# Kernel optimization log

Hardware: AMD Instinct MI355X
Metric: run time of the kernel (lower is better)

## Reference

```python
import jax, jax.numpy as jnp
import numpy as np

N_NODES = 100000
N_EDGES = 3200000
D_IN = 64
D_HID = 64


def _sage_conv(x, src, dst, Wl, bl, Wr, n_nodes):
    # PyG SAGEConv (aggr='mean', root_weight=True):
    #   out = lin_l(mean_{j in N(i)} x_j) + lin_r(x_i)
    msg = x[src]                                              # [E, d] gather
    agg = jax.ops.segment_sum(msg, dst, num_segments=n_nodes) # [N, d] scatter-sum
    cnt = jax.ops.segment_sum(jnp.ones((src.shape[0],), x.dtype), dst,
                              num_segments=n_nodes)           # [N]
    agg = agg / jnp.maximum(cnt, 1.0)[:, None]                # mean (empty -> 0)
    return agg @ Wl.T + bl + x @ Wr.T


def setup_inputs() -> dict:
    key = jax.random.key(0)
    ks = jax.random.split(key, 12)
    x = jax.random.normal(ks[0], (N_NODES, D_IN), dtype=jnp.float32)
    edge_index = jax.random.randint(ks[1], (2, N_EDGES), 0, N_NODES, dtype=jnp.int64)
    s = 1.0 / np.sqrt(D_IN)
    h = 1.0 / np.sqrt(D_HID)
    params = {
        'Wl1': jax.random.uniform(ks[2], (D_HID, D_IN), jnp.float32, -s, s),
        'bl1': jnp.zeros((D_HID,), jnp.float32),
        'Wr1': jax.random.uniform(ks[3], (D_HID, D_IN), jnp.float32, -s, s),
        'Wl2': jax.random.uniform(ks[4], (D_HID, D_HID), jnp.float32, -h, h),
        'bl2': jnp.zeros((D_HID,), jnp.float32),
        'Wr2': jax.random.uniform(ks[5], (D_HID, D_HID), jnp.float32, -h, h),
        'Wl3': jax.random.uniform(ks[6], (D_HID, D_HID), jnp.float32, -h, h),
        'bl3': jnp.zeros((D_HID,), jnp.float32),
        'Wr3': jax.random.uniform(ks[7], (D_HID, D_HID), jnp.float32, -h, h),
        'Wlin': jax.random.uniform(ks[8], (1, D_HID), jnp.float32, -h, h),
        'blin': jnp.zeros((1,), jnp.float32),
    }
    return {'x': x, 'edge_index': edge_index, **params}


def reference(x, edge_index, Wl1, bl1, Wr1, Wl2, bl2, Wr2, Wl3, bl3, Wr3, Wlin, blin):
    src, dst = edge_index[0], edge_index[1]
    n = x.shape[0]
    h = _sage_conv(x, src, dst, Wl1, bl1, Wr1, n)
    h = _sage_conv(h, src, dst, Wl2, bl2, Wr2, n)
    h = _sage_conv(h, src, dst, Wl3, bl3, Wr3, n)
    # global_mean_pool with batch=None -> single graph mean over all nodes
    g = jnp.mean(h, axis=0, keepdims=True)   # [1, D_HID]
    return g @ Wlin.T + blin                 # [1, 1]
```

## Files before the change

kernel.cpp:

```cpp
#include <hip/hip_runtime.h>
#include <stdint.h>

#define D 64
#define PNBLK 512
#define NBMAX 400
#define CAPS 16
#define CAPD 32
#define XPB 512
#define XPST 272

__device__ __forceinline__ uint32_t rup8(uint32_t v) { return (v + 7u) & ~7u; }

__global__ void zero_kernel(float* __restrict__ p, int n) {
    int i = blockIdx.x * blockDim.x + threadIdx.x;
    if (i < n) p[i] = 0.0f;
}

__global__ void cnt_kernel(const int* __restrict__ dst, float* __restrict__ cnt, int ne) {
    int i = blockIdx.x * blockDim.x + threadIdx.x;
    if (i < ne) atomicAdd(&cnt[dst[i]], 1.0f);
}
__global__ void scatter_kernel(const int* __restrict__ src, const int* __restrict__ dst,
                               const float* __restrict__ r, float* __restrict__ an, int ne) {
    int i = blockIdx.x * blockDim.x + threadIdx.x;
    if (i < ne) atomicAdd(&an[src[i]], r[dst[i]]);
}
__global__ void r0_kernel(const float* __restrict__ cnt, float* __restrict__ r, int nn) {
    int i = blockIdx.x * blockDim.x + threadIdx.x;
    if (i < nn) r[i] = (1.0f / (float)nn) / fmaxf(cnt[i], 1.0f);
}
__global__ void rdiv_kernel(const float* __restrict__ a, const float* __restrict__ cnt,
                            float* __restrict__ r, int nn) {
    int i = blockIdx.x * blockDim.x + threadIdx.x;
    if (i < nn) r[i] = a[i] / fmaxf(cnt[i], 1.0f);
}


__global__ __launch_bounds__(512) void hist_kernel(
        const int* __restrict__ src, const int* __restrict__ dst,
        uint32_t* __restrict__ blkhistS, uint32_t* __restrict__ blkhistD,
        int ne, int nb, int chunk) {
    __shared__ uint32_t hS[2][NBMAX], hD[2][NBMAX];
    const int T = blockDim.x, tid = threadIdx.x;
    for (int i = tid; i < nb; i += T) { hS[0][i] = 0u; hS[1][i] = 0u; hD[0][i] = 0u; hD[1][i] = 0u; }
    __syncthreads();
    const int cp = tid & 1;
    int beg = blockIdx.x * chunk;
    int end = min(beg + chunk, ne);
    for (int base = beg; base < end; base += T * 4) {
        int e0 = base + tid * 4;
        if (e0 + 3 < end) {
            int4 s4 = *(const int4*)(src + e0);
            int4 d4 = *(const int4*)(dst + e0);
            atomicAdd(&hS[cp][((uint32_t)s4.x) >> 8], 1u);
            atomicAdd(&hS[cp][((uint32_t)s4.y) >> 8], 1u);
            atomicAdd(&hS[cp][((uint32_t)s4.z) >> 8], 1u);
            atomicAdd(&hS[cp][((uint32_t)s4.w) >> 8], 1u);
            atomicAdd(&hD[cp][((uint32_t)d4.x) >> 8], 1u);
            atomicAdd(&hD[cp][((uint32_t)d4.y) >> 8], 1u);
            atomicAdd(&hD[cp][((uint32_t)d4.z) >> 8], 1u);
            atomicAdd(&hD[cp][((uint32_t)d4.w) >> 8], 1u);
        } else {
            for (int k = 0; k < 4; k++) {
                int e = e0 + k;
                if (e < end) {
                    atomicAdd(&hS[cp][((uint32_t)src[e]) >> 8], 1u);
                    atomicAdd(&hD[cp][((uint32_t)dst[e]) >> 8], 1u);
                }
            }
        }
    }
    __syncthreads();
    for (int i = tid; i < nb; i += T) {
        blkhistS[(size_t)blockIdx.x * nb + i] = hS[0][i] + hS[1][i];
        blkhistD[(size_t)blockIdx.x * nb + i] = hD[0][i] + hD[1][i];
    }
}

__global__ __launch_bounds__(64) void reduce_kernel(
        const uint32_t* __restrict__ blkhistS, const uint32_t* __restrict__ blkhistD,
        uint32_t* __restrict__ totS, uint32_t* __restrict__ totD, int nb) {
    int which = (blockIdx.x >= nb) ? 1 : 0;
    int b = blockIdx.x - which * nb;
    const uint32_t* bh = which ? blkhistD : blkhistS;
    uint32_t* to       = which ? totD : totS;
    int lane = threadIdx.x;
    uint32_t s = 0;
    #pragma unroll
    for (int j = 0; j < PNBLK / 64; j++) {
        uint32_t c = bh[(size_t)(lane + j * 64) * nb + b];
        s += which ? c : rup8(c);
    }
    #pragma unroll
    for (int off = 32; off; off >>= 1) s += __shfl_down(s, off);
    if (lane == 0) to[b] = s;
}

__global__ __launch_bounds__(512) void scan_kernel(
        const uint32_t* __restrict__ totS, const uint32_t* __restrict__ totD,
        uint32_t* __restrict__ bstartS, uint32_t* __restrict__ bstartD,
        float* __restrict__ X, int nb) {
    const int isS = (blockIdx.x == 0);
    const uint32_t* to = isS ? totS : totD;
    uint32_t* bs       = isS ? bstartS : bstartD;
    const int tid = threadIdx.x;
    if (!isS && tid < 4 * D + 2) X[tid] = 0.0f;
    uint32_t tot = (tid < nb) ? to[tid] : 0u;
    int lane = tid & 63, wid = tid >> 6;
    uint32_t incl = tot;
    #pragma unroll
    for (int off = 1; off < 64; off <<= 1) {
        uint32_t nbr = __shfl_up(incl, off, 64);
        if (lane >= off) incl += nbr;
    }
    __shared__ uint32_t wsum[8];
    if (lane == 63) wsum[wid] = incl;
    __syncthreads();
    if (wid == 0 && lane < 8) {
        uint32_t w = wsum[lane], wi = w;
        #pragma unroll
        for (int off = 1; off < 8; off <<= 1) {
            uint32_t nbr = __shfl_up(wi, off, 8);
            if (lane >= off) wi += nbr;
        }
        wsum[lane] = wi - w;
    }
    __syncthreads();
    uint32_t excl = incl - tot + wsum[wid];
    if (tid < nb) bs[tid] = excl;
    if (tid == nb - 1) bs[nb] = excl + tot;
}

__global__ __launch_bounds__(64) void offsets_kernel(
        const uint32_t* __restrict__ blkhistS, const uint32_t* __restrict__ blkhistD,
        const uint32_t* __restrict__ bstartS, const uint32_t* __restrict__ bstartD,
        uint32_t* __restrict__ offsS, uint32_t* __restrict__ offsD, int nb) {
    int which = (blockIdx.x >= nb) ? 1 : 0;
    int b = blockIdx.x - which * nb;
    const uint32_t* bh = which ? blkhistD : blkhistS;
    const uint32_t* bs = which ? bstartD  : bstartS;
    uint32_t* of       = which ? offsD    : offsS;
    int lane = threadIdx.x;
    const int K = PNBLK / 64;
    uint32_t v[K];
    uint32_t s = 0;
    int base = lane * K;
    #pragma unroll
    for (int k = 0; k < K; k++) {
        uint32_t c = bh[(size_t)(base + k) * nb + b];
        v[k] = which ? c : rup8(c);
        s += v[k];
    }
    uint32_t inc = s;
    #pragma unroll
    for (int off = 1; off < 64; off <<= 1) {
        uint32_t nbr = __shfl_up(inc, off, 64);
        if (lane >= off) inc += nbr;
    }
    uint32_t run = bs[b] + (inc - s);
    #pragma unroll
    for (int k = 0; k < K; k++) { of[(size_t)(base + k) * nb + b] = run; run += v[k]; }
}

__global__ __launch_bounds__(512) void place_kernel(
        const int* __restrict__ src, const int* __restrict__ dst,
        const uint32_t* __restrict__ offsS, const uint32_t* __restrict__ offsD,
        uint32_t* __restrict__ sortedS, uint8_t* __restrict__ sortedD,
        int ne, int nb, int chunk, uint32_t sentinel) {
    __shared__ uint32_t stS[NBMAX * CAPS];
    __shared__ uint8_t  stD[NBMAX * CAPD];
    __shared__ uint32_t pendS[NBMAX], pendD[NBMAX];
    __shared__ uint32_t gposS[NBMAX], gposD[NBMAX];
    __shared__ int again;
    const int T = blockDim.x, tid = threadIdx.x;
    for (int i = tid; i < nb; i += T) {
        pendS[i] = 0u; pendD[i] = 0u;
        gposS[i] = offsS[(size_t)blockIdx.x * nb + i];
        gposD[i] = offsD[(size_t)blockIdx.x * nb + i];
    }
    __syncthreads();
    int beg = blockIdx.x * chunk;
    int end = min(beg + chunk, ne);
    for (int base = beg; base < end; base += T * 4) {
        uint32_t vS[4]; uint8_t vD[4]; int bS[4], bD[4]; bool hS[4], hD[4];
        int e0 = base + tid * 4;
        if (e0 + 3 < end) {
            int4 s4 = *(const int4*)(src + e0);
            int4 d4 = *(const int4*)(dst + e0);
            int sv[4] = {s4.x, s4.y, s4.z, s4.w};
            int dv[4] = {d4.x, d4.y, d4.z, d4.w};
            #pragma unroll
            for (int k = 0; k < 4; k++) {
                uint32_t s = (uint32_t)sv[k], d = (uint32_t)dv[k];
                bS[k] = s >> 8; vS[k] = ((s & 255u) << 17) | d;
                bD[k] = d >> 8; vD[k] = (uint8_t)(d & 255u);
                hS[k] = true; hD[k] = true;
            }
        } else {
            #pragma unroll
            for (int k = 0; k < 4; k++) {
                int e = e0 + k;
                bool ok = e < end;
                hS[k] = ok; hD[k] = ok;
                if (ok) {
                    uint32_t s = (uint32_t)src[e], d = (uint32_t)dst[e];
                    bS[k] = s >> 8; vS[k] = ((s & 255u) << 17) | d;
                    bD[k] = d >> 8; vD[k] = (uint8_t)(d & 255u);
                } else { bS[k] = 0; bD[k] = 0; vS[k] = 0; vD[k] = 0; }
            }
        }
        while (true) {
            if (tid == 0) again = 0;
            __syncthreads();
            #pragma unroll
            for (int k = 0; k < 4; k++) {
                if (hS[k]) {
                    uint32_t p = atomicAdd(&pendS[bS[k]], 1u);
                    if (p < CAPS) { stS[bS[k] * CAPS + p] = vS[k]; hS[k] = false; }
                }
                if (hD[k]) {
                    uint32_t p = atomicAdd(&pendD[bD[k]], 1u);
                    if (p < CAPD) { stD[bD[k] * CAPD + p] = vD[k]; hD[k] = false; }
                }
            }
            if (hS[0] | hS[1] | hS[2] | hS[3] | hD[0] | hD[1] | hD[2] | hD[3]) again = 1;
            __syncthreads();
            for (int bb = tid; bb < nb; bb += T) {
                uint32_t n = min(pendS[bb], (uint32_t)CAPS);
                if (n == CAPS) {
                    uint32_t g = gposS[bb];
                    uint4* dstp = (uint4*)(sortedS + g);
                    const uint4* srcp = (const uint4*)(stS + bb * CAPS);
                    dstp[0] = srcp[0]; dstp[1] = srcp[1];
                    dstp[2] = srcp[2]; dstp[3] = srcp[3];
                    gposS[bb] = g + CAPS;
                    pendS[bb] = 0u;
                } else pendS[bb] = n;
                n = min(pendD[bb], (uint32_t)CAPD);
                if (n == CAPD) {
                    uint32_t g = gposD[bb];
                    #pragma unroll
                    for (int k = 0; k < CAPD; k++) sortedD[g + k] = stD[bb * CAPD + k];
                    gposD[bb] = g + CAPD;
                    pendD[bb] = 0u;
                } else pendD[bb] = n;
            }
            __syncthreads();
            const int cont = again;
            __syncthreads();
            if (!cont) break;
        }
    }
    for (int bb = tid; bb < nb; bb += T) {
        uint32_t n = pendS[bb];
        if (n > 0) {
            uint32_t g = gposS[bb];
            uint32_t m = rup8(n);
            uint32_t tmp[CAPS];
            for (uint32_t k = 0; k < m; k++) tmp[k] = (k < n) ? stS[bb * CAPS + k] : sentinel;
            for (uint32_t k = 0; k < m; k += 8) {
                uint4* dstp = (uint4*)(sortedS + g + k);
                dstp[0] = *(const uint4*)(tmp + k);
                dstp[1] = *(const uint4*)(tmp + k + 4);
            }
        }
        uint32_t nD = pendD[bb], gD = gposD[bb];
        for (uint32_t k = 0; k < nD; k++) sortedD[gD + k] = stD[bb * CAPD + k];
    }
}

__global__ __launch_bounds__(512) void cntb_kernel(
        const uint8_t* __restrict__ sortedD, const uint32_t* __restrict__ bstartD,
        float* __restrict__ cnt, float* __restrict__ rA, float* __restrict__ rB,
        int nn, float invN) {
    int b = blockIdx.x, tid = threadIdx.x;
    __shared__ uint32_t c[2][256];
    ((uint32_t*)c)[tid] = 0u;
    __syncthreads();
    const int cp = tid & 1;
    uint32_t beg = bstartD[b], end = bstartD[b + 1];
    for (uint32_t e = beg + tid; e < end; e += 512) atomicAdd(&c[cp][sortedD[e]], 1u);
    __syncthreads();
    if (b == 0 && tid == 0) { rA[nn] = 0.0f; rB[nn] = 0.0f; }
    int v = b * 256 + tid;
    if (tid < 256 && v < nn) {
        float cf = (float)(c[0][tid] + c[1][tid]);
        cnt[v] = cf;
        rA[v] = invN / fmaxf(cf, 1.0f);
    }
}

__global__ __launch_bounds__(512) void scatb_kernel(
        const uint32_t* __restrict__ sortedS, const uint32_t* __restrict__ bstartS,
        const float* __restrict__ rin, const float* __restrict__ cnt,
        float* __restrict__ aout, float* __restrict__ rout, int nn) {
    int b = blockIdx.x, tid = threadIdx.x;
    __shared__ float acc[2][256];
    ((float*)acc)[tid] = 0.0f;
    __syncthreads();
    const int cp = tid & 1;
    uint32_t beg = bstartS[b], end = bstartS[b + 1];
    for (uint32_t e = beg + tid * 4; e < end; e += 512 * 4) {
        uint4 p = *(const uint4*)(sortedS + e);
        atomicAdd(&acc[cp][p.x >> 17], rin[p.x & 0x1FFFFu]);
        atomicAdd(&acc[cp][p.y >> 17], rin[p.y & 0x1FFFFu]);
        atomicAdd(&acc[cp][p.z >> 17], rin[p.z & 0x1FFFFu]);
        atomicAdd(&acc[cp][p.w >> 17], rin[p.w & 0x1FFFFu]);
    }
    __syncthreads();
    int v = b * 256 + tid;
    if (tid < 256 && v < nn) {
        float a = acc[0][tid] + acc[1][tid];
        aout[v] = a;
        if (rout) rout[v] = a / fmaxf(cnt[v], 1.0f);
    }
}

__global__ __launch_bounds__(256) void xpass_kernel(
        const float* __restrict__ x,
        const float* __restrict__ a1, const float* __restrict__ a2,
        const float* __restrict__ a3, float* __restrict__ Xpart, int nn) {
    const int tid = threadIdx.x;
    const int cg = tid & 15;
    const int rs = tid >> 4;
    float4 c0 = {0,0,0,0}, c1 = {0,0,0,0}, c2 = {0,0,0,0}, c3 = {0,0,0,0};
    float ss1 = 0.f, ss2 = 0.f;
    for (int i = blockIdx.x * 16 + rs; i < nn; i += gridDim.x * 16) {
        float4 xv = *(const float4*)(x + (size_t)i * D + cg * 4);
        float w1 = a1[i], w2 = a2[i], w3 = a3[i];
        c0.x += xv.x; c0.y += xv.y; c0.z += xv.z; c0.w += xv.w;
        c1.x = fmaf(w1, xv.x, c1.x); c1.y = fmaf(w1, xv.y, c1.y);
        c1.z = fmaf(w1, xv.z, c1.z); c1.w = fmaf(w1, xv.w, c1.w);
        c2.x = fmaf(w2, xv.x, c2.x); c2.y = fmaf(w2, xv.y, c2.y);
        c2.z = fmaf(w2, xv.z, c2.z); c2.w = fmaf(w2, xv.w, c2.w);
        c3.x = fmaf(w3, xv.x, c3.x); c3.y = fmaf(w3, xv.y, c3.y);
        c3.z = fmaf(w3, xv.z, c3.z); c3.w = fmaf(w3, xv.w, c3.w);
        if (cg == 0) { ss1 += w1; ss2 += w2; }
    }
    __shared__ float4 sm[4][16][16];
    __shared__ float sms1[16], sms2[16];
    sm[0][rs][cg] = c0; sm[1][rs][cg] = c1; sm[2][rs][cg] = c2; sm[3][rs][cg] = c3;
    if (cg == 0) { sms1[rs] = ss1; sms2[rs] = ss2; }
    __syncthreads();
    for (int s = 8; s; s >>= 1) {
        if (rs < s) {
            #pragma unroll
            for (int k = 0; k < 4; k++) {
                float4 a = sm[k][rs][cg], b = sm[k][rs + s][cg];
                a.x += b.x; a.y += b.y; a.z += b.z; a.w += b.w;
                sm[k][rs][cg] = a;
            }
            if (cg == 0) { sms1[rs] += sms1[rs + s]; sms2[rs] += sms2[rs + s]; }
        }
        __syncthreads();
    }
    float* outp = Xpart + (size_t)blockIdx.x * XPST;
    {
        int k = tid >> 6, col = tid & 63;
        outp[tid] = ((const float*)&sm[k][0][col >> 2])[col & 3];
    }
    if (tid == 0) outp[256] = sms1[0];
    if (tid == 1) outp[257] = sms2[0];
}

__global__ __launch_bounds__(64) void xreduce_kernel(
        const float* __restrict__ Xpart, float* __restrict__ X, int nxb) {
    int j = blockIdx.x;
    int lane = threadIdx.x;
    float s = 0.f;
    for (int b = lane; b < nxb; b += 64) s += Xpart[(size_t)b * XPST + j];
    #pragma unroll
    for (int off = 32; off; off >>= 1) s += __shfl_down(s, off);
    if (lane == 0) X[j] = s;
}

__global__ __launch_bounds__(256) void final_kernel(const float* __restrict__ X,
    const float* __restrict__ Wl1, const float* __restrict__ bl1, const float* __restrict__ Wr1,
    const float* __restrict__ Wl2, const float* __restrict__ bl2, const float* __restrict__ Wr2,
    const float* __restrict__ Wl3, const float* __restrict__ bl3, const float* __restrict__ Wr3,
    const float* __restrict__ Wlin, const float* __restrict__ blin,
    float* __restrict__ out, int nn) {
    const int tid = threadIdx.x;
    const int t = tid >> 2, q = tid & 3, c0 = q * 16;
    __shared__ float X1[D], X2[D], X3[D], X4[D];
    __shared__ float m1u[D], m1a1[D], m1a2[D], m2u[D], m2a1[D];
    __shared__ float sred[4];
    if (tid < 64)       X1[tid]       = X[tid] * (1.0f / (float)nn);
    else if (tid < 128) X2[tid - 64]  = X[tid];
    else if (tid < 192) X3[tid - 128] = X[tid];
    else                X4[tid - 192] = X[tid];
    const float s1 = X[4 * D], s2 = X[4 * D + 1];
    __syncthreads();

    float dl2 = 0.f, dl3 = 0.f, dl4 = 0.f, dr1 = 0.f, dr2 = 0.f, dr3 = 0.f;
    #pragma unroll
    for (int k = 0; k < 16; k++) {
        int c = c0 + k;
        float wl = Wl1[t * D + c], wr = Wr1[t * D + c];
        dl2 = fmaf(wl, X2[c], dl2); dl3 = fmaf(wl, X3[c], dl3); dl4 = fmaf(wl, X4[c], dl4);
        dr1 = fmaf(wr, X1[c], dr1); dr2 = fmaf(wr, X2[c], dr2); dr3 = fmaf(wr, X3[c], dr3);
    }
    #define RED4(v) { v += __shfl_down(v, 2, 4); v += __shfl_down(v, 1, 4); }
    RED4(dl2) RED4(dl3) RED4(dl4) RED4(dr1) RED4(dr2) RED4(dr3)
    if (q == 0) {
        m1u[t]  = dl2 + bl1[t]      + dr1;
        m1a1[t] = dl3 + bl1[t] * s1 + dr2;
        m1a2[t] = dl4 + bl1[t] * s2 + dr3;
    }
    __syncthreads();

    float el1 = 0.f, el2 = 0.f, er0 = 0.f, er1 = 0.f;
    #pragma unroll
    for (int k = 0; k < 16; k++) {
        int c = c0 + k;
        float wl = Wl2[t * D + c], wr = Wr2[t * D + c];
        el1 = fmaf(wl, m1a1[c], el1); el2 = fmaf(wl, m1a2[c], el2);
        er0 = fmaf(wr, m1u[c],  er0); er1 = fmaf(wr, m1a1[c], er1);
    }
    RED4(el1) RED4(el2) RED4(er0) RED4(er1)
    if (q == 0) {
        m2u[t]  = el1 + bl2[t]      + er0;
        m2a1[t] = el2 + bl2[t] * s1 + er1;
    }
    __syncthreads();

    float fl = 0.f, fr = 0.f;
    #pragma unroll
    for (int k = 0; k < 16; k++) {
        int c = c0 + k;
        fl = fmaf(Wl3[t * D + c], m2a1[c], fl);
        fr = fmaf(Wr3[t * D + c], m2u[c],  fr);
    }
    RED4(fl) RED4(fr)
    float contrib = 0.f;
    if (q == 0) contrib = Wlin[t] * (fl + bl3[t] + fr);
    #pragma unroll
    for (int off = 32; off; off >>= 1) contrib += __shfl_down(contrib, off);
    if ((tid & 63) == 0) sred[tid >> 6] = contrib;
    __syncthreads();
    if (tid == 0) out[0] = sred[0] + sred[1] + sred[2] + sred[3] + blin[0];
}

extern "C" void kernel_launch(void* const* d_in, const int* in_sizes, int n_in,
                              void* d_out, int out_size, void* d_ws, size_t ws_size,
                              hipStream_t stream) {
    const float* x    = (const float*)d_in[0];
    const int*   ei   = (const int*)d_in[1];
    const float* Wl1  = (const float*)d_in[2];
    const float* bl1  = (const float*)d_in[3];
    const float* Wr1  = (const float*)d_in[4];
    const float* Wl2  = (const float*)d_in[5];
    const float* bl2  = (const float*)d_in[6];
    const float* Wr2  = (const float*)d_in[7];
    const float* Wl3  = (const float*)d_in[8];
    const float* bl3  = (const float*)d_in[9];
    const float* Wr3  = (const float*)d_in[10];
    const float* Wlin = (const float*)d_in[11];
    const float* blin = (const float*)d_in[12];
    float* out = (float*)d_out;

    const int nn = in_sizes[0] / D;
    const int ne = in_sizes[1] / 2;
    const int* srcIdx = ei;
    const int* dstIdx = ei + ne;
    const int nb = (nn + 255) >> 8;

    char* base = (char*)d_ws;
    size_t cur = 0;
    auto alloc = [&](size_t bytes) -> void* {
        void* p = base + cur;
        cur = (cur + bytes + 255) & ~(size_t)255;
        return p;
    };
    float*    cnt      = (float*)alloc((size_t)nn * 4);
    float*    a1       = (float*)alloc((size_t)nn * 4);
    float*    a2       = (float*)alloc((size_t)nn * 4);
    float*    a3       = (float*)alloc((size_t)nn * 4);
    float*    rA       = (float*)alloc((size_t)(nn + 1) * 4);
    float*    rB       = (float*)alloc((size_t)(nn + 1) * 4);
    float*    X        = (float*)alloc((4 * D + 2) * 4);
    float*    Xpart    = (float*)alloc((size_t)XPB * XPST * 4);
    size_t    zend     = cur;
    uint32_t* blkhistS = (uint32_t*)alloc((size_t)PNBLK * nb * 4);
    uint32_t* blkhistD = (uint32_t*)alloc((size_t)PNBLK * nb * 4);
    uint32_t* offsS    = (uint32_t*)alloc((size_t)PNBLK * nb * 4);
    uint32_t* offsD    = (uint32_t*)alloc((size_t)PNBLK * nb * 4);
    uint32_t* bstartS  = (uint32_t*)alloc((size_t)(nb + 1) * 4);
    uint32_t* bstartD  = (uint32_t*)alloc((size_t)(nb + 1) * 4);
    uint32_t* totS     = (uint32_t*)alloc((size_t)nb * 4);
    uint32_t* totD     = (uint32_t*)alloc((size_t)nb * 4);
    uint32_t* sortedS  = (uint32_t*)alloc(((size_t)ne + (size_t)PNBLK * nb * 7) * 4);
    uint8_t*  sortedD  = (uint8_t*)alloc((size_t)ne);
    const size_t need = cur;

    const int B = 256;
    if (need <= ws_size && nn <= 131071 && nb <= NBMAX) {
        const int chunk = ((ne + PNBLK - 1) / PNBLK + 3) & ~3;
        hipLaunchKernelGGL(hist_kernel, dim3(PNBLK), dim3(512), 0, stream,
                           srcIdx, dstIdx, blkhistS, blkhistD, ne, nb, chunk);
        hipLaunchKernelGGL(reduce_kernel, dim3(2 * nb), dim3(64), 0, stream,
                           blkhistS, blkhistD, totS, totD, nb);
        hipLaunchKernelGGL(scan_kernel, dim3(2), dim3(512), 0, stream,
                           totS, totD, bstartS, bstartD, X, nb);
        hipLaunchKernelGGL(offsets_kernel, dim3(2 * nb), dim3(64), 0, stream,
                           blkhistS, blkhistD, bstartS, bstartD, offsS, offsD, nb);
        hipLaunchKernelGGL(place_kernel, dim3(PNBLK), dim3(512), 0, stream,
                           srcIdx, dstIdx, offsS, offsD, sortedS, sortedD, ne, nb, chunk,
                           (uint32_t)nn);
        hipLaunchKernelGGL(cntb_kernel, dim3(nb), dim3(512), 0, stream,
                           sortedD, bstartD, cnt, rA, rB, nn, 1.0f / (float)nn);
        hipLaunchKernelGGL(scatb_kernel, dim3(nb), dim3(512), 0, stream,
                           sortedS, bstartS, rA, cnt, a1, rB, nn);
        hipLaunchKernelGGL(scatb_kernel, dim3(nb), dim3(512), 0, stream,
                           sortedS, bstartS, rB, cnt, a2, rA, nn);
        hipLaunchKernelGGL(scatb_kernel, dim3(nb), dim3(512), 0, stream,
                           sortedS, bstartS, rA, cnt, a3, (float*)nullptr, nn);
    } else {
        const int zn = (int)(zend / 4);
        hipLaunchKernelGGL(zero_kernel, dim3((zn + B - 1) / B), dim3(B), 0, stream, (float*)d_ws, zn);
        hipLaunchKernelGGL(cnt_kernel,  dim3((ne + B - 1) / B), dim3(B), 0, stream, dstIdx, cnt, ne);
        hipLaunchKernelGGL(r0_kernel,   dim3((nn + B - 1) / B), dim3(B), 0, stream, cnt, rA, nn);
        hipLaunchKernelGGL(scatter_kernel, dim3((ne + B - 1) / B), dim3(B), 0, stream, srcIdx, dstIdx, rA, a1, ne);
        hipLaunchKernelGGL(rdiv_kernel, dim3((nn + B - 1) / B), dim3(B), 0, stream, a1, cnt, rA, nn);
        hipLaunchKernelGGL(scatter_kernel, dim3((ne + B - 1) / B), dim3(B), 0, stream, srcIdx, dstIdx, rA, a2, ne);
        hipLaunchKernelGGL(rdiv_kernel, dim3((nn + B - 1) / B), dim3(B), 0, stream, a2, cnt, rA, nn);
        hipLaunchKernelGGL(scatter_kernel, dim3((ne + B - 1) / B), dim3(B), 0, stream, srcIdx, dstIdx, rA, a3, ne);
    }

    hipLaunchKernelGGL(xpass_kernel, dim3(XPB), dim3(B), 0, stream, x, a1, a2, a3, Xpart, nn);
    hipLaunchKernelGGL(xreduce_kernel, dim3(4 * D + 2), dim3(64), 0, stream, Xpart, X, XPB);
    hipLaunchKernelGGL(final_kernel, dim3(1), dim3(B), 0, stream, X,
                       Wl1, bl1, Wr1, Wl2, bl2, Wr2, Wl3, bl3, Wr3, Wlin, blin, out, nn);
}
```

Baseline: 158.7 us.

## Fuse count and three scatter passes into one persistent kernel with grid barriers

Merges the per-bucket count kernel and the three scatter kernels into a single kernel that separates phases with a global atomic barrier, and folds the reduce and offsets kernels into one by adding bucket starts later in place_kernel. LDS histogram copies grow from two to four to cut atomic contention. This removes several kernel launches and their gaps, but the software grid barrier needs every block to be resident at once, which risks deadlock if occupancy is insufficient, and adds spin overhead.

```diff
diff --git a/kernel.cpp b/kernel.cpp
--- a/kernel.cpp
+++ b/kernel.cpp
@@ -40,11 +40,14 @@
         const int* __restrict__ src, const int* __restrict__ dst,
         uint32_t* __restrict__ blkhistS, uint32_t* __restrict__ blkhistD,
         int ne, int nb, int chunk) {
-    __shared__ uint32_t hS[2][NBMAX], hD[2][NBMAX];
+    __shared__ uint32_t hS[4][NBMAX], hD[4][NBMAX];
     const int T = blockDim.x, tid = threadIdx.x;
-    for (int i = tid; i < nb; i += T) { hS[0][i] = 0u; hS[1][i] = 0u; hD[0][i] = 0u; hD[1][i] = 0u; }
-    __syncthreads();
-    const int cp = tid & 1;
+    for (int i = tid; i < nb; i += T) {
+        hS[0][i] = 0u; hS[1][i] = 0u; hS[2][i] = 0u; hS[3][i] = 0u;
+        hD[0][i] = 0u; hD[1][i] = 0u; hD[2][i] = 0u; hD[3][i] = 0u;
+    }
+    __syncthreads();
+    const int cp = tid & 3;
     int beg = blockIdx.x * chunk;
     int end = min(beg + chunk, ne);
     for (int base = beg; base < end; base += T * 4) {
@@ -72,39 +75,55 @@
     }
     __syncthreads();
     for (int i = tid; i < nb; i += T) {
-        blkhistS[(size_t)blockIdx.x * nb + i] = hS[0][i] + hS[1][i];
-        blkhistD[(size_t)blockIdx.x * nb + i] = hD[0][i] + hD[1][i];
-    }
-}
-
-__global__ __launch_bounds__(64) void reduce_kernel(
+        blkhistS[(size_t)blockIdx.x * nb + i] = hS[0][i] + hS[1][i] + hS[2][i] + hS[3][i];
+        blkhistD[(size_t)blockIdx.x * nb + i] = hD[0][i] + hD[1][i] + hD[2][i] + hD[3][i];
+    }
+}
+
+__global__ __launch_bounds__(64) void reduceoffs_kernel(
         const uint32_t* __restrict__ blkhistS, const uint32_t* __restrict__ blkhistD,
+        uint32_t* __restrict__ offsS, uint32_t* __restrict__ offsD,
         uint32_t* __restrict__ totS, uint32_t* __restrict__ totD, int nb) {
     int which = (blockIdx.x >= nb) ? 1 : 0;
     int b = blockIdx.x - which * nb;
     const uint32_t* bh = which ? blkhistD : blkhistS;
-    uint32_t* to       = which ? totD : totS;
+    uint32_t* of       = which ? offsD    : offsS;
+    uint32_t* to       = which ? totD     : totS;
     int lane = threadIdx.x;
+    const int K = PNBLK / 64;
+    uint32_t v[K];
     uint32_t s = 0;
-    #pragma unroll
-    for (int j = 0; j < PNBLK / 64; j++) {
-        uint32_t c = bh[(size_t)(lane + j * 64) * nb + b];
-        s += which ? c : rup8(c);
-    }
-    #pragma unroll
-    for (int off = 32; off; off >>= 1) s += __shfl_down(s, off);
-    if (lane == 0) to[b] = s;
+    int base = lane * K;
+    #pragma unroll
+    for (int k = 0; k < K; k++) {
+        uint32_t c = bh[(size_t)(base + k) * nb + b];
+        v[k] = which ? c : rup8(c);
+        s += v[k];
+    }
+    uint32_t inc = s;
+    #pragma unroll
+    for (int off = 1; off < 64; off <<= 1) {
+        uint32_t nbr = __shfl_up(inc, off, 64);
+        if (lane >= off) inc += nbr;
+    }
+    uint32_t run = inc - s;
+    #pragma unroll
+    for (int k = 0; k < K; k++) { of[(size_t)(base + k) * nb + b] = run; run += v[k]; }
+    if (lane == 63) to[b] = inc;
 }
 
 __global__ __launch_bounds__(512) void scan_kernel(
         const uint32_t* __restrict__ totS, const uint32_t* __restrict__ totD,
         uint32_t* __restrict__ bstartS, uint32_t* __restrict__ bstartD,
-        float* __restrict__ X, int nb) {
+        float* __restrict__ X, uint32_t* __restrict__ bar, int nb) {
     const int isS = (blockIdx.x == 0);
     const uint32_t* to = isS ? totS : totD;
     uint32_t* bs       = isS ? bstartS : bstartD;
     const int tid = threadIdx.x;
-    if (!isS && tid < 4 * D + 2) X[tid] = 0.0f;
+    if (!isS) {
+        if (tid < 4 * D + 2) X[tid] = 0.0f;
+        if (tid >= 500 && tid < 504) bar[tid - 500] = 0u;
+    }
     uint32_t tot = (tid < nb) ? to[tid] : 0u;
     int lane = tid & 63, wid = tid >> 6;
     uint32_t incl = tot;
@@ -131,40 +150,10 @@
     if (tid == nb - 1) bs[nb] = excl + tot;
 }
 
-__global__ __launch_bounds__(64) void offsets_kernel(
-        const uint32_t* __restrict__ blkhistS, const uint32_t* __restrict__ blkhistD,
-        const uint32_t* __restrict__ bstartS, const uint32_t* __restrict__ bstartD,
-        uint32_t* __restrict__ offsS, uint32_t* __restrict__ offsD, int nb) {
-    int which = (blockIdx.x >= nb) ? 1 : 0;
-    int b = blockIdx.x - which * nb;
-    const uint32_t* bh = which ? blkhistD : blkhistS;
-    const uint32_t* bs = which ? bstartD  : bstartS;
-    uint32_t* of       = which ? offsD    : offsS;
-    int lane = threadIdx.x;
-    const int K = PNBLK / 64;
-    uint32_t v[K];
-    uint32_t s = 0;
-    int base = lane * K;
-    #pragma unroll
-    for (int k = 0; k < K; k++) {
-        uint32_t c = bh[(size_t)(base + k) * nb + b];
-        v[k] = which ? c : rup8(c);
-        s += v[k];
-    }
-    uint32_t inc = s;
-    #pragma unroll
-    for (int off = 1; off < 64; off <<= 1) {
-        uint32_t nbr = __shfl_up(inc, off, 64);
-        if (lane >= off) inc += nbr;
-    }
-    uint32_t run = bs[b] + (inc - s);
-    #pragma unroll
-    for (int k = 0; k < K; k++) { of[(size_t)(base + k) * nb + b] = run; run += v[k]; }
-}
-
 __global__ __launch_bounds__(512) void place_kernel(
         const int* __restrict__ src, const int* __restrict__ dst,
         const uint32_t* __restrict__ offsS, const uint32_t* __restrict__ offsD,
+        const uint32_t* __restrict__ bstartS, const uint32_t* __restrict__ bstartD,
         uint32_t* __restrict__ sortedS, uint8_t* __restrict__ sortedD,
         int ne, int nb, int chunk, uint32_t sentinel) {
     __shared__ uint32_t stS[NBMAX * CAPS];
@@ -175,8 +164,8 @@
     const int T = blockDim.x, tid = threadIdx.x;
     for (int i = tid; i < nb; i += T) {
         pendS[i] = 0u; pendD[i] = 0u;
-        gposS[i] = offsS[(size_t)blockIdx.x * nb + i];
-        gposD[i] = offsD[(size_t)blockIdx.x * nb + i];
+        gposS[i] = bstartS[i] + offsS[(size_t)blockIdx.x * nb + i];
+        gposD[i] = bstartD[i] + offsD[(size_t)blockIdx.x * nb + i];
     }
     __syncthreads();
     int beg = blockIdx.x * chunk;
@@ -269,51 +258,73 @@
     }
 }
 
-__global__ __launch_bounds__(512) void cntb_kernel(
+__device__ __forceinline__ void grid_barrier(uint32_t* bar, uint32_t nblocks) {
+    __syncthreads();
+    if (threadIdx.x == 0) {
+        __threadfence();
+        atomicAdd(bar, 1u);
+        while (atomicAdd(bar, 0u) < nblocks) {
+            __builtin_amdgcn_s_sleep(8);
+        }
+        __threadfence();
+    }
+    __syncthreads();
+}
+
+__global__ __launch_bounds__(512, 4) void adjoint_kernel(
+        const uint32_t* __restrict__ sortedS, const uint32_t* __restrict__ bstartS,
         const uint8_t* __restrict__ sortedD, const uint32_t* __restrict__ bstartD,
-        float* __restrict__ cnt, float* __restrict__ rA, float* __restrict__ rB,
-        int nn, float invN) {
-    int b = blockIdx.x, tid = threadIdx.x;
-    __shared__ uint32_t c[2][256];
-    ((uint32_t*)c)[tid] = 0u;
-    __syncthreads();
-    const int cp = tid & 1;
-    uint32_t beg = bstartD[b], end = bstartD[b + 1];
-    for (uint32_t e = beg + tid; e < end; e += 512) atomicAdd(&c[cp][sortedD[e]], 1u);
-    __syncthreads();
+        float* __restrict__ rA, float* __restrict__ rB,
+        float* __restrict__ a1, float* __restrict__ a2, float* __restrict__ a3,
+        uint32_t* __restrict__ bar, int nn, float invN, int nblocks) {
+    const int b = blockIdx.x, tid = threadIdx.x;
+    __shared__ uint32_t lds[4 * 256];
+    float* ldsf = (float*)lds;
+    const int cp = tid & 3;
+    const int v = b * 256 + tid;
+
+    lds[tid] = 0u; lds[512 + tid] = 0u;
+    __syncthreads();
+    {
+        uint32_t beg = bstartD[b], end = bstartD[b + 1];
+        for (uint32_t e = beg + tid; e < end; e += 512)
+            atomicAdd(&lds[cp * 256 + sortedD[e]], 1u);
+    }
+    __syncthreads();
+    float myCnt = 1.0f;
+    if (tid < 256) {
+        float cf = (float)(lds[tid] + lds[256 + tid] + lds[512 + tid] + lds[768 + tid]);
+        myCnt = fmaxf(cf, 1.0f);
+        if (v < nn) rA[v] = invN / myCnt;
+    }
     if (b == 0 && tid == 0) { rA[nn] = 0.0f; rB[nn] = 0.0f; }
-    int v = b * 256 + tid;
-    if (tid < 256 && v < nn) {
-        float cf = (float)(c[0][tid] + c[1][tid]);
-        cnt[v] = cf;
-        rA[v] = invN / fmaxf(cf, 1.0f);
-    }
-}
-
-__global__ __launch_bounds__(512) void scatb_kernel(
-        const uint32_t* __restrict__ sortedS, const uint32_t* __restrict__ bstartS,
-        const float* __restrict__ rin, const float* __restrict__ cnt,
-        float* __restrict__ aout, float* __restrict__ rout, int nn) {
-    int b = blockIdx.x, tid = threadIdx.x;
-    __shared__ float acc[2][256];
-    ((float*)acc)[tid] = 0.0f;
-    __syncthreads();
-    const int cp = tid & 1;
-    uint32_t beg = bstartS[b], end = bstartS[b + 1];
-    for (uint32_t e = beg + tid * 4; e < end; e += 512 * 4) {
-        uint4 p = *(const uint4*)(sortedS + e);
-        atomicAdd(&acc[cp][p.x >> 17], rin[p.x & 0x1FFFFu]);
-        atomicAdd(&acc[cp][p.y >> 17], rin[p.y & 0x1FFFFu]);
-        atomicAdd(&acc[cp][p.z >> 17], rin[p.z & 0x1FFFFu]);
-        atomicAdd(&acc[cp][p.w >> 17], rin[p.w & 0x1FFFFu]);
-    }
-    __syncthreads();
-    int v = b * 256 + tid;
-    if (tid < 256 && v < nn) {
-        float a = acc[0][tid] + acc[1][tid];
-        aout[v] = a;
-        if (rout) rout[v] = a / fmaxf(cnt[v], 1.0f);
-    }
+    grid_barrier(bar + 0, (uint32_t)nblocks);
+
+    const uint32_t sbeg = bstartS[b], send = bstartS[b + 1];
+    #define SCAT_PHASE(RIN, AOUT, ROUT)                                          \
+    {                                                                            \
+        lds[tid] = 0u; lds[512 + tid] = 0u;                                      \
+        __syncthreads();                                                         \
+        for (uint32_t e = sbeg + tid * 4; e < send; e += 512 * 4) {              \
+            uint4 p = *(const uint4*)(sortedS + e);                              \
+            atomicAdd(&ldsf[cp * 256 + (p.x >> 17)], RIN[p.x & 0x1FFFFu]);       \
+            atomicAdd(&ldsf[cp * 256 + (p.y >> 17)], RIN[p.y & 0x1FFFFu]);       \
+            atomicAdd(&ldsf[cp * 256 + (p.z >> 17)], RIN[p.z & 0x1FFFFu]);       \
+            atomicAdd(&ldsf[cp * 256 + (p.w >> 17)], RIN[p.w & 0x1FFFFu]);       \
+        }                                                                        \
+        __syncthreads();                                                         \
+        if (tid < 256 && v < nn) {                                               \
+            float a = ldsf[tid] + ldsf[256 + tid] + ldsf[512 + tid] + ldsf[768 + tid]; \
+            AOUT[v] = a;                                                         \
+            if (ROUT) ((float*)ROUT)[v] = a / myCnt;                             \
+        }                                                                        \
+    }
+    SCAT_PHASE(rA, a1, rB)
+    grid_barrier(bar + 1, (uint32_t)nblocks);
+    SCAT_PHASE(rB, a2, rA)
+    grid_barrier(bar + 2, (uint32_t)nblocks);
+    SCAT_PHASE(rA, a3, ((float*)nullptr))
+    #undef SCAT_PHASE
 }
 
 __global__ __launch_bounds__(256) void xpass_kernel(
@@ -481,6 +492,7 @@
     float*    X        = (float*)alloc((4 * D + 2) * 4);
     float*    Xpart    = (float*)alloc((size_t)XPB * XPST * 4);
     size_t    zend     = cur;
+    uint32_t* bar      = (uint32_t*)alloc(4 * 4);
     uint32_t* blkhistS = (uint32_t*)alloc((size_t)PNBLK * nb * 4);
     uint32_t* blkhistD = (uint32_t*)alloc((size_t)PNBLK * nb * 4);
     uint32_t* offsS    = (uint32_t*)alloc((size_t)PNBLK * nb * 4);
@@ -494,27 +506,20 @@
     const size_t need = cur;
 
     const int B = 256;
-    if (need <= ws_size && nn <= 131071 && nb <= NBMAX) {
+    if (need <= ws_size && nn <= 131071 && nb <= NBMAX && nb <= 512) {
         const int chunk = ((ne + PNBLK - 1) / PNBLK + 3) & ~3;
         hipLaunchKernelGGL(hist_kernel, dim3(PNBLK), dim3(512), 0, stream,
                            srcIdx, dstIdx, blkhistS, blkhistD, ne, nb, chunk);
-        hipLaunchKernelGGL(reduce_kernel, dim3(2 * nb), dim3(64), 0, stream,
-                           blkhistS, blkhistD, totS, totD, nb);
+        hipLaunchKernelGGL(reduceoffs_kernel, dim3(2 * nb), dim3(64), 0, stream,
+                           blkhistS, blkhistD, offsS, offsD, totS, totD, nb);
         hipLaunchKernelGGL(scan_kernel, dim3(2), dim3(512), 0, stream,
-                           totS, totD, bstartS, bstartD, X, nb);
-        hipLaunchKernelGGL(offsets_kernel, dim3(2 * nb), dim3(64), 0, stream,
-                           blkhistS, blkhistD, bstartS, bstartD, offsS, offsD, nb);
+                           totS, totD, bstartS, bstartD, X, bar, nb);
         hipLaunchKernelGGL(place_kernel, dim3(PNBLK), dim3(512), 0, stream,
-                           srcIdx, dstIdx, offsS, offsD, sortedS, sortedD, ne, nb, chunk,
-                           (uint32_t)nn);
-        hipLaunchKernelGGL(cntb_kernel, dim3(nb), dim3(512), 0, stream,
-                           sortedD, bstartD, cnt, rA, rB, nn, 1.0f / (float)nn);
-        hipLaunchKernelGGL(scatb_kernel, dim3(nb), dim3(512), 0, stream,
-                           sortedS, bstartS, rA, cnt, a1, rB, nn);
-        hipLaunchKernelGGL(scatb_kernel, dim3(nb), dim3(512), 0, stream,
-                           sortedS, bstartS, rB, cnt, a2, rA, nn);
-        hipLaunchKernelGGL(scatb_kernel, dim3(nb), dim3(512), 0, stream,
-                           sortedS, bstartS, rA, cnt, a3, (float*)nullptr, nn);
+                           srcIdx, dstIdx, offsS, offsD, bstartS, bstartD,
+                           sortedS, sortedD, ne, nb, chunk, (uint32_t)nn);
+        hipLaunchKernelGGL(adjoint_kernel, dim3(nb), dim3(512), 0, stream,
+                           sortedS, bstartS, sortedD, bstartD, rA, rB, a1, a2, a3,
+                           bar, nn, 1.0f / (float)nn, nb);
     } else {
         const int zn = (int)(zend / 4);
         hipLaunchKernelGGL(zero_kernel, dim3((zn + B - 1) / B), dim3(B), 0, stream, (float*)d_ws, zn);
```

New measurement: 262.3 us. 1.65x slower.

## Fuse last scatter with x-pass, merge reduce/offsets, widen histogram copies

Applied to the files above, without the earlier changes.

The third scatter pass now runs inside a new scatx kernel that also does the per-node x weighted reduction for its bucket of 256 nodes, so the a3 array never goes through global memory. The separate xpass kernel and its launch are removed on the fast path. The reduce and offsets kernels become one kernel that computes relative offsets, and place adds the bucket start. The histogram kernel uses four shared-memory copies instead of two to cut atomic contention. In exchange, the x pass is now spread over only nb blocks instead of XPB, and the added offsets kernel writes must land before place reads them.

```diff
diff --git a/kernel.cpp b/kernel.cpp
--- a/kernel.cpp
+++ b/kernel.cpp
@@ -35,16 +35,66 @@
     if (i < nn) r[i] = a[i] / fmaxf(cnt[i], 1.0f);
 }
 
+__global__ __launch_bounds__(256) void xpass_kernel(
+        const float* __restrict__ x,
+        const float* __restrict__ a1, const float* __restrict__ a2,
+        const float* __restrict__ a3, float* __restrict__ Xpart, int nn) {
+    const int tid = threadIdx.x;
+    const int cg = tid & 15;
+    const int rs = tid >> 4;
+    float4 c0 = {0,0,0,0}, c1 = {0,0,0,0}, c2 = {0,0,0,0}, c3 = {0,0,0,0};
+    float ss1 = 0.f, ss2 = 0.f;
+    for (int i = blockIdx.x * 16 + rs; i < nn; i += gridDim.x * 16) {
+        float4 xv = *(const float4*)(x + (size_t)i * D + cg * 4);
+        float w1 = a1[i], w2 = a2[i], w3 = a3[i];
+        c0.x += xv.x; c0.y += xv.y; c0.z += xv.z; c0.w += xv.w;
+        c1.x = fmaf(w1, xv.x, c1.x); c1.y = fmaf(w1, xv.y, c1.y);
+        c1.z = fmaf(w1, xv.z, c1.z); c1.w = fmaf(w1, xv.w, c1.w);
+        c2.x = fmaf(w2, xv.x, c2.x); c2.y = fmaf(w2, xv.y, c2.y);
+        c2.z = fmaf(w2, xv.z, c2.z); c2.w = fmaf(w2, xv.w, c2.w);
+        c3.x = fmaf(w3, xv.x, c3.x); c3.y = fmaf(w3, xv.y, c3.y);
+        c3.z = fmaf(w3, xv.z, c3.z); c3.w = fmaf(w3, xv.w, c3.w);
+        if (cg == 0) { ss1 += w1; ss2 += w2; }
+    }
+    __shared__ float4 sm[4][16][16];
+    __shared__ float sms1[16], sms2[16];
+    sm[0][rs][cg] = c0; sm[1][rs][cg] = c1; sm[2][rs][cg] = c2; sm[3][rs][cg] = c3;
+    if (cg == 0) { sms1[rs] = ss1; sms2[rs] = ss2; }
+    __syncthreads();
+    for (int s = 8; s; s >>= 1) {
+        if (rs < s) {
+            #pragma unroll
+            for (int k = 0; k < 4; k++) {
+                float4 a = sm[k][rs][cg], b = sm[k][rs + s][cg];
+                a.x += b.x; a.y += b.y; a.z += b.z; a.w += b.w;
+                sm[k][rs][cg] = a;
+            }
+            if (cg == 0) { sms1[rs] += sms1[rs + s]; sms2[rs] += sms2[rs + s]; }
+        }
+        __syncthreads();
+    }
+    float* outp = Xpart + (size_t)blockIdx.x * XPST;
+    {
+        int k = tid >> 6, col = tid & 63;
+        outp[tid] = ((const float*)&sm[k][0][col >> 2])[col & 3];
+    }
+    if (tid == 0) outp[256] = sms1[0];
+    if (tid == 1) outp[257] = sms2[0];
+}
+
 
 __global__ __launch_bounds__(512) void hist_kernel(
         const int* __restrict__ src, const int* __restrict__ dst,
         uint32_t* __restrict__ blkhistS, uint32_t* __restrict__ blkhistD,
         int ne, int nb, int chunk) {
-    __shared__ uint32_t hS[2][NBMAX], hD[2][NBMAX];
+    __shared__ uint32_t hS[4][NBMAX], hD[4][NBMAX];
     const int T = blockDim.x, tid = threadIdx.x;
-    for (int i = tid; i < nb; i += T) { hS[0][i] = 0u; hS[1][i] = 0u; hD[0][i] = 0u; hD[1][i] = 0u; }
-    __syncthreads();
-    const int cp = tid & 1;
+    for (int i = tid; i < nb; i += T) {
+        hS[0][i] = 0u; hS[1][i] = 0u; hS[2][i] = 0u; hS[3][i] = 0u;
+        hD[0][i] = 0u; hD[1][i] = 0u; hD[2][i] = 0u; hD[3][i] = 0u;
+    }
+    __syncthreads();
+    const int cp = tid & 3;
     int beg = blockIdx.x * chunk;
     int end = min(beg + chunk, ne);
     for (int base = beg; base < end; base += T * 4) {
@@ -72,39 +122,50 @@
     }
     __syncthreads();
     for (int i = tid; i < nb; i += T) {
-        blkhistS[(size_t)blockIdx.x * nb + i] = hS[0][i] + hS[1][i];
-        blkhistD[(size_t)blockIdx.x * nb + i] = hD[0][i] + hD[1][i];
-    }
-}
-
-__global__ __launch_bounds__(64) void reduce_kernel(
+        blkhistS[(size_t)blockIdx.x * nb + i] = hS[0][i] + hS[1][i] + hS[2][i] + hS[3][i];
+        blkhistD[(size_t)blockIdx.x * nb + i] = hD[0][i] + hD[1][i] + hD[2][i] + hD[3][i];
+    }
+}
+
+__global__ __launch_bounds__(64) void reduceoffs_kernel(
         const uint32_t* __restrict__ blkhistS, const uint32_t* __restrict__ blkhistD,
+        uint32_t* __restrict__ offsS, uint32_t* __restrict__ offsD,
         uint32_t* __restrict__ totS, uint32_t* __restrict__ totD, int nb) {
     int which = (blockIdx.x >= nb) ? 1 : 0;
     int b = blockIdx.x - which * nb;
     const uint32_t* bh = which ? blkhistD : blkhistS;
-    uint32_t* to       = which ? totD : totS;
+    uint32_t* of       = which ? offsD    : offsS;
+    uint32_t* to       = which ? totD     : totS;
     int lane = threadIdx.x;
+    const int K = PNBLK / 64;
+    uint32_t v[K];
     uint32_t s = 0;
-    #pragma unroll
-    for (int j = 0; j < PNBLK / 64; j++) {
-        uint32_t c = bh[(size_t)(lane + j * 64) * nb + b];
-        s += which ? c : rup8(c);
-    }
-    #pragma unroll
-    for (int off = 32; off; off >>= 1) s += __shfl_down(s, off);
-    if (lane == 0) to[b] = s;
+    int base = lane * K;
+    #pragma unroll
+    for (int k = 0; k < K; k++) {
+        uint32_t c = bh[(size_t)(base + k) * nb + b];
+        v[k] = which ? c : rup8(c);
+        s += v[k];
+    }
+    uint32_t inc = s;
+    #pragma unroll
+    for (int off = 1; off < 64; off <<= 1) {
+        uint32_t nbr = __shfl_up(inc, off, 64);
+        if (lane >= off) inc += nbr;
+    }
+    uint32_t run = inc - s;
+    #pragma unroll
+    for (int k = 0; k < K; k++) { of[(size_t)(base + k) * nb + b] = run; run += v[k]; }
+    if (lane == 63) to[b] = inc;
 }
 
 __global__ __launch_bounds__(512) void scan_kernel(
         const uint32_t* __restrict__ totS, const uint32_t* __restrict__ totD,
-        uint32_t* __restrict__ bstartS, uint32_t* __restrict__ bstartD,
-        float* __restrict__ X, int nb) {
+        uint32_t* __restrict__ bstartS, uint32_t* __restrict__ bstartD, int nb) {
     const int isS = (blockIdx.x == 0);
     const uint32_t* to = isS ? totS : totD;
     uint32_t* bs       = isS ? bstartS : bstartD;
     const int tid = threadIdx.x;
-    if (!isS && tid < 4 * D + 2) X[tid] = 0.0f;
     uint32_t tot = (tid < nb) ? to[tid] : 0u;
     int lane = tid & 63, wid = tid >> 6;
     uint32_t incl = tot;
@@ -131,40 +192,10 @@
     if (tid == nb - 1) bs[nb] = excl + tot;
 }
 
-__global__ __launch_bounds__(64) void offsets_kernel(
-        const uint32_t* __restrict__ blkhistS, const uint32_t* __restrict__ blkhistD,
-        const uint32_t* __restrict__ bstartS, const uint32_t* __restrict__ bstartD,
-        uint32_t* __restrict__ offsS, uint32_t* __restrict__ offsD, int nb) {
-    int which = (blockIdx.x >= nb) ? 1 : 0;
-    int b = blockIdx.x - which * nb;
-    const uint32_t* bh = which ? blkhistD : blkhistS;
-    const uint32_t* bs = which ? bstartD  : bstartS;
-    uint32_t* of       = which ? offsD    : offsS;
-    int lane = threadIdx.x;
-    const int K = PNBLK / 64;
-    uint32_t v[K];
-    uint32_t s = 0;
-    int base = lane * K;
-    #pragma unroll
-    for (int k = 0; k < K; k++) {
-        uint32_t c = bh[(size_t)(base + k) * nb + b];
-        v[k] = which ? c : rup8(c);
-        s += v[k];
-    }
-    uint32_t inc = s;
-    #pragma unroll
-    for (int off = 1; off < 64; off <<= 1) {
-        uint32_t nbr = __shfl_up(inc, off, 64);
-        if (lane >= off) inc += nbr;
-    }
-    uint32_t run = bs[b] + (inc - s);
-    #pragma unroll
-    for (int k = 0; k < K; k++) { of[(size_t)(base + k) * nb + b] = run; run += v[k]; }
-}
-
 __global__ __launch_bounds__(512) void place_kernel(
         const int* __restrict__ src, const int* __restrict__ dst,
         const uint32_t* __restrict__ offsS, const uint32_t* __restrict__ offsD,
+        const uint32_t* __restrict__ bstartS, const uint32_t* __restrict__ bstartD,
         uint32_t* __restrict__ sortedS, uint8_t* __restrict__ sortedD,
         int ne, int nb, int chunk, uint32_t sentinel) {
     __shared__ uint32_t stS[NBMAX * CAPS];
@@ -175,8 +206,8 @@
     const int T = blockDim.x, tid = threadIdx.x;
     for (int i = tid; i < nb; i += T) {
         pendS[i] = 0u; pendD[i] = 0u;
-        gposS[i] = offsS[(size_t)blockIdx.x * nb + i];
-        gposD[i] = offsD[(size_t)blockIdx.x * nb + i];
+        gposS[i] = bstartS[i] + offsS[(size_t)blockIdx.x * nb + i];
+        gposD[i] = bstartD[i] + offsD[(size_t)blockIdx.x * nb + i];
     }
     __syncthreads();
     int beg = blockIdx.x * chunk;
@@ -316,18 +347,35 @@
     }
 }
 
-__global__ __launch_bounds__(256) void xpass_kernel(
-        const float* __restrict__ x,
+__global__ __launch_bounds__(512) void scatx_kernel(
+        const uint32_t* __restrict__ sortedS, const uint32_t* __restrict__ bstartS,
+        const float* __restrict__ rin, const float* __restrict__ x,
         const float* __restrict__ a1, const float* __restrict__ a2,
-        const float* __restrict__ a3, float* __restrict__ Xpart, int nn) {
-    const int tid = threadIdx.x;
-    const int cg = tid & 15;
-    const int rs = tid >> 4;
+        float* __restrict__ Xpart, int nn) {
+    const int b = blockIdx.x, tid = threadIdx.x;
+    __shared__ float acc[2][256];
+    ((float*)acc)[tid] = 0.0f;
+    __syncthreads();
+    const int cp = tid & 1;
+    uint32_t beg = bstartS[b], end = bstartS[b + 1];
+    for (uint32_t e = beg + tid * 4; e < end; e += 512 * 4) {
+        uint4 p = *(const uint4*)(sortedS + e);
+        atomicAdd(&acc[cp][p.x >> 17], rin[p.x & 0x1FFFFu]);
+        atomicAdd(&acc[cp][p.y >> 17], rin[p.y & 0x1FFFFu]);
+        atomicAdd(&acc[cp][p.z >> 17], rin[p.z & 0x1FFFFu]);
+        atomicAdd(&acc[cp][p.w >> 17], rin[p.w & 0x1FFFFu]);
+    }
+    __syncthreads();
+    const int cg = tid & 15, rs = tid >> 4;
     float4 c0 = {0,0,0,0}, c1 = {0,0,0,0}, c2 = {0,0,0,0}, c3 = {0,0,0,0};
     float ss1 = 0.f, ss2 = 0.f;
-    for (int i = blockIdx.x * 16 + rs; i < nn; i += gridDim.x * 16) {
-        float4 xv = *(const float4*)(x + (size_t)i * D + cg * 4);
-        float w1 = a1[i], w2 = a2[i], w3 = a3[i];
+    const int vbase = b * 256;
+    for (int r = rs; r < 256; r += 32) {
+        int v = vbase + r;
+        if (v >= nn) break;
+        float4 xv = *(const float4*)(x + (size_t)v * D + cg * 4);
+        float w1 = a1[v], w2 = a2[v];
+        float w3 = acc[0][r] + acc[1][r];
         c0.x += xv.x; c0.y += xv.y; c0.z += xv.z; c0.w += xv.w;
         c1.x = fmaf(w1, xv.x, c1.x); c1.y = fmaf(w1, xv.y, c1.y);
         c1.z = fmaf(w1, xv.z, c1.z); c1.w = fmaf(w1, xv.w, c1.w);
@@ -337,25 +385,25 @@
         c3.z = fmaf(w3, xv.z, c3.z); c3.w = fmaf(w3, xv.w, c3.w);
         if (cg == 0) { ss1 += w1; ss2 += w2; }
     }
-    __shared__ float4 sm[4][16][16];
-    __shared__ float sms1[16], sms2[16];
+    __shared__ float4 sm[4][32][16];
+    __shared__ float sms1[32], sms2[32];
     sm[0][rs][cg] = c0; sm[1][rs][cg] = c1; sm[2][rs][cg] = c2; sm[3][rs][cg] = c3;
     if (cg == 0) { sms1[rs] = ss1; sms2[rs] = ss2; }
     __syncthreads();
-    for (int s = 8; s; s >>= 1) {
+    for (int s = 16; s; s >>= 1) {
         if (rs < s) {
             #pragma unroll
             for (int k = 0; k < 4; k++) {
-                float4 a = sm[k][rs][cg], b = sm[k][rs + s][cg];
-                a.x += b.x; a.y += b.y; a.z += b.z; a.w += b.w;
+                float4 a = sm[k][rs][cg], bb = sm[k][rs + s][cg];
+                a.x += bb.x; a.y += bb.y; a.z += bb.z; a.w += bb.w;
                 sm[k][rs][cg] = a;
             }
             if (cg == 0) { sms1[rs] += sms1[rs + s]; sms2[rs] += sms2[rs + s]; }
         }
         __syncthreads();
     }
-    float* outp = Xpart + (size_t)blockIdx.x * XPST;
-    {
+    float* outp = Xpart + (size_t)b * XPST;
+    if (tid < 256) {
         int k = tid >> 6, col = tid & 63;
         outp[tid] = ((const float*)&sm[k][0][col >> 2])[col & 3];
     }
@@ -498,23 +546,23 @@
         const int chunk = ((ne + PNBLK - 1) / PNBLK + 3) & ~3;
         hipLaunchKernelGGL(hist_kernel, dim3(PNBLK), dim3(512), 0, stream,
                            srcIdx, dstIdx, blkhistS, blkhistD, ne, nb, chunk);
-        hipLaunchKernelGGL(reduce_kernel, dim3(2 * nb), dim3(64), 0, stream,
-                           blkhistS, blkhistD, totS, totD, nb);
+        hipLaunchKernelGGL(reduceoffs_kernel, dim3(2 * nb), dim3(64), 0, stream,
+                           blkhistS, blkhistD, offsS, offsD, totS, totD, nb);
         hipLaunchKernelGGL(scan_kernel, dim3(2), dim3(512), 0, stream,
-                           totS, totD, bstartS, bstartD, X, nb);
-        hipLaunchKernelGGL(offsets_kernel, dim3(2 * nb), dim3(64), 0, stream,
-                           blkhistS, blkhistD, bstartS, bstartD, offsS, offsD, nb);
+                           totS, totD, bstartS, bstartD, nb);
         hipLaunchKernelGGL(place_kernel, dim3(PNBLK), dim3(512), 0, stream,
-                           srcIdx, dstIdx, offsS, offsD, sortedS, sortedD, ne, nb, chunk,
-                           (uint32_t)nn);
+                           srcIdx, dstIdx, offsS, offsD, bstartS, bstartD,
+                           sortedS, sortedD, ne, nb, chunk, (uint32_t)nn);
         hipLaunchKernelGGL(cntb_kernel, dim3(nb), dim3(512), 0, stream,
                            sortedD, bstartD, cnt, rA, rB, nn, 1.0f / (float)nn);
         hipLaunchKernelGGL(scatb_kernel, dim3(nb), dim3(512), 0, stream,
                            sortedS, bstartS, rA, cnt, a1, rB, nn);
         hipLaunchKernelGGL(scatb_kernel, dim3(nb), dim3(512), 0, stream,
                            sortedS, bstartS, rB, cnt, a2, rA, nn);
-        hipLaunchKernelGGL(scatb_kernel, dim3(nb), dim3(512), 0, stream,
-                           sortedS, bstartS, rA, cnt, a3, (float*)nullptr, nn);
+        hipLaunchKernelGGL(scatx_kernel, dim3(nb), dim3(512), 0, stream,
+                           sortedS, bstartS, rA, x, a1, a2, Xpart, nn);
+        hipLaunchKernelGGL(xreduce_kernel, dim3(4 * D + 2), dim3(64), 0, stream,
+                           Xpart, X, nb);
     } else {
         const int zn = (int)(zend / 4);
         hipLaunchKernelGGL(zero_kernel, dim3((zn + B - 1) / B), dim3(B), 0, stream, (float*)d_ws, zn);
@@ -525,10 +573,10 @@
         hipLaunchKernelGGL(scatter_kernel, dim3((ne + B - 1) / B), dim3(B), 0, stream, srcIdx, dstIdx, rA, a2, ne);
         hipLaunchKernelGGL(rdiv_kernel, dim3((nn + B - 1) / B), dim3(B), 0, stream, a2, cnt, rA, nn);
         hipLaunchKernelGGL(scatter_kernel, dim3((ne + B - 1) / B), dim3(B), 0, stream, srcIdx, dstIdx, rA, a3, ne);
-    }
-
-    hipLaunchKernelGGL(xpass_kernel, dim3(XPB), dim3(B), 0, stream, x, a1, a2, a3, Xpart, nn);
-    hipLaunchKernelGGL(xreduce_kernel, dim3(4 * D + 2), dim3(64), 0, stream, Xpart, X, XPB);
+        hipLaunchKernelGGL(xpass_kernel, dim3(XPB), dim3(B), 0, stream, x, a1, a2, a3, Xpart, nn);
+        hipLaunchKernelGGL(xreduce_kernel, dim3(4 * D + 2), dim3(64), 0, stream, Xpart, X, XPB);
+    }
+
     hipLaunchKernelGGL(final_kernel, dim3(1), dim3(B), 0, stream, X,
                        Wl1, bl1, Wr1, Wl2, bl2, Wr2, Wl3, bl3, Wr3, Wlin, blin, out, nn);
 }
```

Measured after the change: 153.3 us. -3.4%, faster.
